# Kernel optimization log

Hardware: AMD Instinct MI355X
Metric: run time of the kernel (lower is better)

Reference implementation:

```python
import jax, jax.numpy as jnp
import numpy as np

jax.config.update("jax_enable_x64", True)

# --- static config (matches init_kwargs) ---
L = 6            # voxel_level_num
F = 8            # feature_dim
T = 524288       # per-level feature table size
B = 4194304      # buffer_size (hash table size)
N = 1048576      # number of query points
LEAF = 0.25      # leaf_voxel_size
UP = 2.0         # up_scale_factor

PRIMES = jnp.array([73856093, 19349669, 83492791], dtype=jnp.int64)
# corner offsets, z varies fastest (same order as torch self.steps)
STEPS = jnp.array([[0,0,0],[0,0,1],[0,1,0],[0,1,1],
                   [1,0,0],[1,0,1],[1,1,0],[1,1,1]], dtype=jnp.float32)


def setup_inputs() -> dict:
    key = jax.random.key(0)
    k1, k2, k3, k4 = jax.random.split(key, 4)
    query_points = jax.random.uniform(k1, (N, 3), dtype=jnp.float32) * 50.0
    features = 0.01 * jax.random.normal(k2, (L, T, F), dtype=jnp.float32)
    idx = jax.random.randint(k3, (L, B), 0, T, dtype=jnp.int64)
    empty = jax.random.uniform(k4, (L, B)) < 0.2
    feature_indexs = jnp.where(empty, jnp.int64(-1), idx)
    return {"query_points": query_points, "features": features,
            "feature_indexs": feature_indexs}


def _trilinear_coeffs(d):
    # d: [N,3] fractional coords in the cell; order matches STEPS (z fastest)
    tx, ty, tz = d[:, 0], d[:, 1], d[:, 2]
    return jnp.stack([
        (1-tx)*(1-ty)*(1-tz), (1-tx)*(1-ty)*tz,
        (1-tx)*ty*(1-tz),     (1-tx)*ty*tz,
        tx*(1-ty)*(1-tz),     tx*(1-ty)*tz,
        tx*ty*(1-tz),         tx*ty*tz,
    ], axis=1)  # [N,8]


def reference(query_points, features, feature_indexs):
    out = jnp.zeros((query_points.shape[0], F), dtype=query_points.dtype)
    for i in range(L):  # small fixed level loop (structurally distinct resolutions)
        res = LEAF * (UP ** i)
        scaled = query_points / res                      # [N,3]
        base = jnp.floor(scaled)
        corners = (base[:, None, :] + STEPS[None]).astype(jnp.int64)  # [N,8,3]
        keys = jnp.mod((corners * PRIMES).sum(-1), B)    # [N,8] spatial hash
        idx = feature_indexs[i][keys]                    # [N,8] gather, -1 = empty
        valid = idx.min(axis=1) > -1                     # [N] all 8 corners allocated
        coeffs = _trilinear_coeffs(scaled - base)        # [N,8]
        feats = features[i][jnp.clip(idx, 0, T - 1)]     # [N,8,F] gather
        level = jnp.einsum('nkf,nk->nf', feats, coeffs)  # trilinear interp
        out = out + jnp.where(valid[:, None], level, jnp.zeros((), out.dtype))
    return out
```

## Files before the change

### kernel.cpp

```cpp
#include <hip/hip_runtime.h>


static constexpr int      NPTS  = 1048576;
static constexpr int      LVLS  = 6;
static constexpr int      NF    = 8;
static constexpr int      TTAB  = 524288;
static constexpr unsigned BTAB  = 4194304u;
static constexpr unsigned BMASK = BTAB - 1u;
static constexpr unsigned P0 = 73856093u, P1 = 19349669u, P2 = 83492791u;

static constexpr int NBIN = 4096;
static constexpr int SB   = 256;
static constexpr int PPB  = NPTS / SB;
static constexpr int ITER = PPB / 256;
static constexpr int BCAP = 512;

typedef float f4 __attribute__((ext_vector_type(4)));

__device__ __forceinline__ void nhv_point(
    float qx, float qy, float qz,
    const float* __restrict__ feat, const int* __restrict__ fidx, float acc[NF])
{
    float    fx[LVLS], fy[LVLS], fz[LVLS];
    unsigned h[LVLS];
#pragma unroll
    for (int i = 0; i < LVLS; ++i) {
        const float inv = 4.0f / (float)(1 << i);
        const float sx = qx * inv, sy = qy * inv, sz = qz * inv;
        const float bx = floorf(sx), by = floorf(sy), bz = floorf(sz);
        fx[i] = sx - bx; fy[i] = sy - by; fz[i] = sz - bz;
        h[i] = (unsigned)(int)bx * P0 + (unsigned)(int)by * P1 + (unsigned)(int)bz * P2;
    }

    int id[LVLS][8];
#pragma unroll
    for (int i = 0; i < LVLS; ++i) {
        const int* __restrict__ tab = fidx + (size_t)i * BTAB;
#pragma unroll
        for (int k = 0; k < 8; ++k) {
            unsigned key = h[i];
            if (k & 4) key += P0;
            if (k & 2) key += P1;
            if (k & 1) key += P2;
            id[i][k] = tab[key & BMASK];
        }
    }

#pragma unroll
    for (int f = 0; f < NF; ++f) acc[f] = 0.0f;

#pragma unroll
    for (int i = 0; i < LVLS; ++i) {
        int mn = id[i][0];
#pragma unroll
        for (int k = 1; k < 8; ++k) mn = min(mn, id[i][k]);
        if (mn > -1) {
            const float wxv[2] = {1.0f - fx[i], fx[i]};
            const float wyv[2] = {1.0f - fy[i], fy[i]};
            const float wzv[2] = {1.0f - fz[i], fz[i]};
            const float* __restrict__ fb = feat + (size_t)i * (TTAB * NF);
#pragma unroll
            for (int k = 0; k < 8; ++k) {
                const float c = wxv[(k >> 2) & 1] * wyv[(k >> 1) & 1] * wzv[k & 1];
                const float4* p = (const float4*)(fb + (size_t)id[i][k] * NF);
                const float4 lo = p[0];
                const float4 hi = p[1];
                acc[0] += c * lo.x; acc[1] += c * lo.y;
                acc[2] += c * lo.z; acc[3] += c * lo.w;
                acc[4] += c * hi.x; acc[5] += c * hi.y;
                acc[6] += c * hi.z; acc[7] += c * hi.w;
            }
        }
    }
}

__device__ __forceinline__ unsigned expand4(unsigned v) {
    return (v & 1u) | ((v & 2u) << 2) | ((v & 4u) << 4) | ((v & 8u) << 6);
}
__device__ __forceinline__ unsigned bin_of(float x, float y, float z) {
    unsigned bx = min(15u, (unsigned)(int)(x * 0.32f));
    unsigned by = min(15u, (unsigned)(int)(y * 0.32f));
    unsigned bz = min(15u, (unsigned)(int)(z * 0.32f));
    return expand4(bx) | (expand4(by) << 1) | (expand4(bz) << 2);
}
__device__ __forceinline__ unsigned expand10(unsigned v) {
    v = (v | (v << 16)) & 0x030000FFu;
    v = (v | (v << 8))  & 0x0300F00Fu;
    v = (v | (v << 4))  & 0x030C30C3u;
    v = (v | (v << 2))  & 0x09249249u;
    return v;
}
__device__ __forceinline__ unsigned morton30(float x, float y, float z) {
    unsigned ux = min(1023u, (unsigned)(int)(x * 20.48f));
    unsigned uy = min(1023u, (unsigned)(int)(y * 20.48f));
    unsigned uz = min(1023u, (unsigned)(int)(z * 20.48f));
    return expand10(ux) | (expand10(uy) << 1) | (expand10(uz) << 2);
}

__global__ __launch_bounds__(256) void hist_k(const float* __restrict__ qp,
                                              unsigned* __restrict__ hist) {
    __shared__ unsigned lh[NBIN];
    const int b = blockIdx.x, t = threadIdx.x;
    for (int i = t; i < NBIN; i += 256) lh[i] = 0u;
    __syncthreads();
    const int base = b * PPB;
#pragma unroll
    for (int i = 0; i < ITER; ++i) {
        const int p = base + i * 256 + t;
        atomicAdd(&lh[bin_of(qp[3*p], qp[3*p+1], qp[3*p+2])], 1u);
    }
    __syncthreads();
    for (int i = t; i < NBIN; i += 256) hist[(size_t)b * NBIN + i] = lh[i];
}

__global__ __launch_bounds__(256) void colscan_k(unsigned* __restrict__ hist,
                                                 unsigned* __restrict__ binbase) {
    const int bin = blockIdx.x * 256 + threadIdx.x;
    unsigned run = 0;
    for (int b = 0; b < SB; ++b) {
        const unsigned v = hist[(size_t)b * NBIN + bin];
        hist[(size_t)b * NBIN + bin] = run;
        run += v;
    }
    binbase[bin] = run;
}

__global__ __launch_bounds__(256) void binscan_k(unsigned* __restrict__ binbase) {
    __shared__ unsigned tot[256];
    const int t = threadIdx.x;
    unsigned v[16];
    unsigned s = 0;
#pragma unroll
    for (int i = 0; i < 16; ++i) { v[i] = s; s += binbase[t * 16 + i]; }
    tot[t] = s;
    __syncthreads();
    for (int d = 1; d < 256; d <<= 1) {
        const unsigned x = (t >= d) ? tot[t - d] : 0u;
        __syncthreads();
        tot[t] += x;
        __syncthreads();
    }
    const unsigned cb = tot[t] - s;
#pragma unroll
    for (int i = 0; i < 16; ++i) binbase[t * 16 + i] = cb + v[i];
}

__global__ __launch_bounds__(256) void scatter_k(const float* __restrict__ qp,
                                                 const unsigned* __restrict__ hist,
                                                 const unsigned* __restrict__ binbase,
                                                 float4* __restrict__ sorted) {
    __shared__ unsigned cur[NBIN];
    const int b = blockIdx.x, t = threadIdx.x;
    for (int i = t; i < NBIN; i += 256)
        cur[i] = binbase[i] + hist[(size_t)b * NBIN + i];
    __syncthreads();
    const int base = b * PPB;
#pragma unroll
    for (int i = 0; i < ITER; ++i) {
        const int p = base + i * 256 + t;
        const float x = qp[3*p], y = qp[3*p+1], z = qp[3*p+2];
        const unsigned slot = atomicAdd(&cur[bin_of(x, y, z)], 1u);
        sorted[slot] = make_float4(x, y, z, __uint_as_float((unsigned)p));
    }
}

__global__ __launch_bounds__(256) void binsort_k(float4* __restrict__ sorted,
                                                 const unsigned* __restrict__ binbase) {
    __shared__ float4   pts[BCAP];
    __shared__ unsigned key[BCAP];
    __shared__ unsigned short pay[BCAP];

    const int bin   = blockIdx.x;
    const int t     = threadIdx.x;
    const unsigned start = binbase[bin];
    const unsigned end   = (bin < NBIN - 1) ? binbase[bin + 1] : (unsigned)NPTS;
    const int n = (int)(end - start);
    if (n <= 1 || n > BCAP) return;

#pragma unroll
    for (int r = 0; r < BCAP / 256; ++r) {
        const int i = r * 256 + t;
        if (i < n) {
            const float4 p = sorted[start + i];
            pts[i] = p;
            key[i] = morton30(p.x, p.y, p.z);
        } else {
            key[i] = 0xFFFFFFFFu;
        }
        pay[i] = (unsigned short)i;
    }
    __syncthreads();

    for (int k = 2; k <= BCAP; k <<= 1) {
        for (int j = k >> 1; j > 0; j >>= 1) {
#pragma unroll
            for (int r = 0; r < BCAP / 512; ++r) {
                const int tid = r * 256 + t;
                const int i   = ((tid & ~(j - 1)) << 1) | (tid & (j - 1));
                const int p2  = i | j;
                const bool up = ((i & k) == 0);
                const unsigned ka = key[i], kb = key[p2];
                if ((ka > kb) == up) {
                    key[i] = kb; key[p2] = ka;
                    const unsigned short tmp = pay[i]; pay[i] = pay[p2]; pay[p2] = tmp;
                }
            }
            __syncthreads();
        }
    }

#pragma unroll
    for (int r = 0; r < BCAP / 256; ++r) {
        const int i = r * 256 + t;
        if (i < n) sorted[start + i] = pts[pay[i]];
    }
}

__global__ __launch_bounds__(256) void nhv_sorted_k(
    const float4* __restrict__ sp, const float* __restrict__ feat,
    const int* __restrict__ fidx, float* __restrict__ out)
{
    const int nwg = NPTS / 256;
    const int bid = blockIdx.x;
    const int swz = (bid & 7) * (nwg >> 3) + (bid >> 3);
    const int j   = swz * 256 + (int)threadIdx.x;

    const f4 s = __builtin_nontemporal_load((const f4*)sp + j);
    float acc[NF];
    nhv_point(s.x, s.y, s.z, feat, fidx, acc);
    const unsigned n = __float_as_uint(s.w);

    f4* o = (f4*)(out + (size_t)n * NF);
    f4 lo = {acc[0], acc[1], acc[2], acc[3]};
    f4 hi = {acc[4], acc[5], acc[6], acc[7]};
    __builtin_nontemporal_store(lo, o);
    __builtin_nontemporal_store(hi, o + 1);
}

__global__ __launch_bounds__(256) void nhv_direct_k(
    const float* __restrict__ qp, const float* __restrict__ feat,
    const int* __restrict__ fidx, float* __restrict__ out)
{
    const int n = blockIdx.x * 256 + threadIdx.x;
    if (n >= NPTS) return;
    float acc[NF];
    nhv_point(qp[3*n], qp[3*n+1], qp[3*n+2], feat, fidx, acc);
    float4* o = (float4*)(out + (size_t)n * NF);
    o[0] = make_float4(acc[0], acc[1], acc[2], acc[3]);
    o[1] = make_float4(acc[4], acc[5], acc[6], acc[7]);
}

extern "C" void kernel_launch(void* const* d_in, const int* in_sizes, int n_in,
                              void* d_out, int out_size, void* d_ws, size_t ws_size,
                              hipStream_t stream) {
    const float* qp   = (const float*)d_in[0];
    const float* feat = (const float*)d_in[1];
    const int*   fidx = (const int*)d_in[2];
    float*       out  = (float*)d_out;

    const size_t ws_needed = (size_t)NPTS * 16;

    if (ws_size >= ws_needed) {
        unsigned* hist    = (unsigned*)d_out;
        unsigned* binbase = hist + (size_t)SB * NBIN;
        float4*   sorted  = (float4*)d_ws;

        hipLaunchKernelGGL(hist_k,    dim3(SB),   dim3(256), 0, stream, qp, hist);
        hipLaunchKernelGGL(colscan_k, dim3(16),   dim3(256), 0, stream, hist, binbase);
        hipLaunchKernelGGL(binscan_k, dim3(1),    dim3(256), 0, stream, binbase);
        hipLaunchKernelGGL(scatter_k, dim3(SB),   dim3(256), 0, stream, qp, hist, binbase, sorted);
        hipLaunchKernelGGL(binsort_k, dim3(NBIN), dim3(256), 0, stream, sorted, binbase);
        hipLaunchKernelGGL(nhv_sorted_k, dim3(NPTS/256), dim3(256), 0, stream,
                           sorted, feat, fidx, out);
    } else {
        hipLaunchKernelGGL(nhv_direct_k, dim3(NPTS/256), dim3(256), 0, stream,
                           qp, feat, fidx, out);
    }
}
```

Baseline: 223.9 us.

## Add validity bitmap prepass and replace bitonic bin sort with counting sort

A new kernel packs the per-level hash table's -1 markers into a bitmap, 32 slots per word, built freshly on every call. The main kernel first checks corner validity against this compact bitmap and fetches indices and features only for levels where all 8 corners are allocated. This cuts index-table traffic for invalid levels, at the cost of streaming the full 6x4M index table once to build the bitmap. The per-bin bitonic Morton sort is also replaced by a cheaper 64-way counting sort on a coarse octant key, which gives less precise spatial ordering.

```diff
diff --git a/kernel.cpp b/kernel.cpp
--- a/kernel.cpp
+++ b/kernel.cpp
@@ -15,11 +15,33 @@
 static constexpr int ITER = PPB / 256;
 static constexpr int BCAP = 512;
 
+static constexpr int    BMW_L        = BTAB / 32;
+static constexpr size_t SORTED_BYTES = (size_t)NPTS * 16;
+static constexpr size_t BM_BYTES     = (size_t)LVLS * BMW_L * 4;
+
 typedef float f4 __attribute__((ext_vector_type(4)));
-
-__device__ __forceinline__ void nhv_point(
+typedef int   i4 __attribute__((ext_vector_type(4)));
+
+__global__ __launch_bounds__(256) void bmbuild_k(const int* __restrict__ fidx,
+                                                 unsigned* __restrict__ bm) {
+    const int g = blockIdx.x * 256 + threadIdx.x;
+    const i4* p = (const i4*)(fidx + (size_t)g * 32);
+    unsigned w = 0;
+#pragma unroll
+    for (int j = 0; j < 8; ++j) {
+        const i4 v = __builtin_nontemporal_load(p + j);
+        w |= (unsigned)(v.x >= 0) << (4 * j + 0);
+        w |= (unsigned)(v.y >= 0) << (4 * j + 1);
+        w |= (unsigned)(v.z >= 0) << (4 * j + 2);
+        w |= (unsigned)(v.w >= 0) << (4 * j + 3);
+    }
+    bm[g] = w;
+}
+
+__device__ __forceinline__ void nhv_point_bm(
     float qx, float qy, float qz,
-    const float* __restrict__ feat, const int* __restrict__ fidx, float acc[NF])
+    const float* __restrict__ feat, const int* __restrict__ fidx,
+    const unsigned* __restrict__ bm, float acc[NF])
 {
     float    fx[LVLS], fy[LVLS], fz[LVLS];
     unsigned h[LVLS];
@@ -32,6 +54,72 @@
         h[i] = (unsigned)(int)bx * P0 + (unsigned)(int)by * P1 + (unsigned)(int)bz * P2;
     }
 
+    unsigned vmask = 0;
+#pragma unroll
+    for (int i = 0; i < LVLS; ++i) {
+        const unsigned* __restrict__ bl = bm + i * BMW_L;
+        unsigned v = ~0u;
+#pragma unroll
+        for (int k = 0; k < 8; ++k) {
+            unsigned key = h[i];
+            if (k & 4) key += P0;
+            if (k & 2) key += P1;
+            if (k & 1) key += P2;
+            key &= BMASK;
+            v &= (bl[key >> 5] >> (key & 31u));
+        }
+        vmask |= (v & 1u) << i;
+    }
+
+#pragma unroll
+    for (int f = 0; f < NF; ++f) acc[f] = 0.0f;
+
+#pragma unroll
+    for (int i = 0; i < LVLS; ++i) {
+        if (vmask & (1u << i)) {
+            const int* __restrict__ tab = fidx + (size_t)i * BTAB;
+            int id[8];
+#pragma unroll
+            for (int k = 0; k < 8; ++k) {
+                unsigned key = h[i];
+                if (k & 4) key += P0;
+                if (k & 2) key += P1;
+                if (k & 1) key += P2;
+                id[k] = tab[key & BMASK];
+            }
+            const float wxv[2] = {1.0f - fx[i], fx[i]};
+            const float wyv[2] = {1.0f - fy[i], fy[i]};
+            const float wzv[2] = {1.0f - fz[i], fz[i]};
+            const float* __restrict__ fb = feat + (size_t)i * (TTAB * NF);
+#pragma unroll
+            for (int k = 0; k < 8; ++k) {
+                const float c = wxv[(k >> 2) & 1] * wyv[(k >> 1) & 1] * wzv[k & 1];
+                const float4* p = (const float4*)(fb + (size_t)id[k] * NF);
+                const float4 lo = p[0];
+                const float4 hi = p[1];
+                acc[0] += c * lo.x; acc[1] += c * lo.y;
+                acc[2] += c * lo.z; acc[3] += c * lo.w;
+                acc[4] += c * hi.x; acc[5] += c * hi.y;
+                acc[6] += c * hi.z; acc[7] += c * hi.w;
+            }
+        }
+    }
+}
+
+__device__ __forceinline__ void nhv_point(
+    float qx, float qy, float qz,
+    const float* __restrict__ feat, const int* __restrict__ fidx, float acc[NF])
+{
+    float    fx[LVLS], fy[LVLS], fz[LVLS];
+    unsigned h[LVLS];
+#pragma unroll
+    for (int i = 0; i < LVLS; ++i) {
+        const float inv = 4.0f / (float)(1 << i);
+        const float sx = qx * inv, sy = qy * inv, sz = qz * inv;
+        const float bx = floorf(sx), by = floorf(sy), bz = floorf(sz);
+        fx[i] = sx - bx; fy[i] = sy - by; fz[i] = sz - bz;
+        h[i] = (unsigned)(int)bx * P0 + (unsigned)(int)by * P1 + (unsigned)(int)bz * P2;
+    }
     int id[LVLS][8];
 #pragma unroll
     for (int i = 0; i < LVLS; ++i) {
@@ -45,10 +133,8 @@
             id[i][k] = tab[key & BMASK];
         }
     }
-
 #pragma unroll
     for (int f = 0; f < NF; ++f) acc[f] = 0.0f;
-
 #pragma unroll
     for (int i = 0; i < LVLS; ++i) {
         int mn = id[i][0];
@@ -83,19 +169,6 @@
     unsigned bz = min(15u, (unsigned)(int)(z * 0.32f));
     return expand4(bx) | (expand4(by) << 1) | (expand4(bz) << 2);
 }
-__device__ __forceinline__ unsigned expand10(unsigned v) {
-    v = (v | (v << 16)) & 0x030000FFu;
-    v = (v | (v << 8))  & 0x0300F00Fu;
-    v = (v | (v << 4))  & 0x030C30C3u;
-    v = (v | (v << 2))  & 0x09249249u;
-    return v;
-}
-__device__ __forceinline__ unsigned morton30(float x, float y, float z) {
-    unsigned ux = min(1023u, (unsigned)(int)(x * 20.48f));
-    unsigned uy = min(1023u, (unsigned)(int)(y * 20.48f));
-    unsigned uz = min(1023u, (unsigned)(int)(z * 20.48f));
-    return expand10(ux) | (expand10(uy) << 1) | (expand10(uz) << 2);
-}
 
 __global__ __launch_bounds__(256) void hist_k(const float* __restrict__ qp,
                                               unsigned* __restrict__ hist) {
@@ -166,59 +239,54 @@
 
 __global__ __launch_bounds__(256) void binsort_k(float4* __restrict__ sorted,
                                                  const unsigned* __restrict__ binbase) {
-    __shared__ float4   pts[BCAP];
-    __shared__ unsigned key[BCAP];
-    __shared__ unsigned short pay[BCAP];
-
-    const int bin   = blockIdx.x;
-    const int t     = threadIdx.x;
+    __shared__ float4        pts[BCAP];
+    __shared__ unsigned char sk[BCAP];
+    __shared__ unsigned      cnt[64];
+
+    const int bin = blockIdx.x, t = threadIdx.x;
     const unsigned start = binbase[bin];
     const unsigned end   = (bin < NBIN - 1) ? binbase[bin + 1] : (unsigned)NPTS;
     const int n = (int)(end - start);
     if (n <= 1 || n > BCAP) return;
 
+    if (t < 64) cnt[t] = 0u;
+    __syncthreads();
 #pragma unroll
     for (int r = 0; r < BCAP / 256; ++r) {
         const int i = r * 256 + t;
         if (i < n) {
             const float4 p = sorted[start + i];
             pts[i] = p;
-            key[i] = morton30(p.x, p.y, p.z);
-        } else {
-            key[i] = 0xFFFFFFFFu;
-        }
-        pay[i] = (unsigned short)i;
-    }
-    __syncthreads();
-
-    for (int k = 2; k <= BCAP; k <<= 1) {
-        for (int j = k >> 1; j > 0; j >>= 1) {
-#pragma unroll
-            for (int r = 0; r < BCAP / 512; ++r) {
-                const int tid = r * 256 + t;
-                const int i   = ((tid & ~(j - 1)) << 1) | (tid & (j - 1));
-                const int p2  = i | j;
-                const bool up = ((i & k) == 0);
-                const unsigned ka = key[i], kb = key[p2];
-                if ((ka > kb) == up) {
-                    key[i] = kb; key[p2] = ka;
-                    const unsigned short tmp = pay[i]; pay[i] = pay[p2]; pay[p2] = tmp;
-                }
-            }
-            __syncthreads();
-        }
-    }
-
+            const unsigned ux = (unsigned)(int)(p.x * 1.28f) & 3u;
+            const unsigned uy = (unsigned)(int)(p.y * 1.28f) & 3u;
+            const unsigned uz = (unsigned)(int)(p.z * 1.28f) & 3u;
+            const unsigned s = (ux & 1u) | ((uy & 1u) << 1) | ((uz & 1u) << 2)
+                             | ((ux >> 1) << 3) | ((uy >> 1) << 4) | ((uz >> 1) << 5);
+            sk[i] = (unsigned char)s;
+            atomicAdd(&cnt[s], 1u);
+        }
+    }
+    __syncthreads();
+    if (t == 0) {
+        unsigned run = 0;
+#pragma unroll
+        for (int i = 0; i < 64; ++i) { const unsigned v = cnt[i]; cnt[i] = run; run += v; }
+    }
+    __syncthreads();
 #pragma unroll
     for (int r = 0; r < BCAP / 256; ++r) {
         const int i = r * 256 + t;
-        if (i < n) sorted[start + i] = pts[pay[i]];
-    }
-}
-
-__global__ __launch_bounds__(256) void nhv_sorted_k(
+        if (i < n) {
+            const unsigned dest = atomicAdd(&cnt[sk[i]], 1u);
+            sorted[start + dest] = pts[i];
+        }
+    }
+}
+
+__global__ __launch_bounds__(256) void nhv_sorted_bm_k(
     const float4* __restrict__ sp, const float* __restrict__ feat,
-    const int* __restrict__ fidx, float* __restrict__ out)
+    const int* __restrict__ fidx, const unsigned* __restrict__ bm,
+    float* __restrict__ out)
 {
     const int nwg = NPTS / 256;
     const int bid = blockIdx.x;
@@ -227,9 +295,29 @@
 
     const f4 s = __builtin_nontemporal_load((const f4*)sp + j);
     float acc[NF];
+    nhv_point_bm(s.x, s.y, s.z, feat, fidx, bm, acc);
+    const unsigned n = __float_as_uint(s.w);
+
+    f4* o = (f4*)(out + (size_t)n * NF);
+    f4 lo = {acc[0], acc[1], acc[2], acc[3]};
+    f4 hi = {acc[4], acc[5], acc[6], acc[7]};
+    __builtin_nontemporal_store(lo, o);
+    __builtin_nontemporal_store(hi, o + 1);
+}
+
+__global__ __launch_bounds__(256) void nhv_sorted_k(
+    const float4* __restrict__ sp, const float* __restrict__ feat,
+    const int* __restrict__ fidx, float* __restrict__ out)
+{
+    const int nwg = NPTS / 256;
+    const int bid = blockIdx.x;
+    const int swz = (bid & 7) * (nwg >> 3) + (bid >> 3);
+    const int j   = swz * 256 + (int)threadIdx.x;
+
+    const f4 s = __builtin_nontemporal_load((const f4*)sp + j);
+    float acc[NF];
     nhv_point(s.x, s.y, s.z, feat, fidx, acc);
     const unsigned n = __float_as_uint(s.w);
-
     f4* o = (f4*)(out + (size_t)n * NF);
     f4 lo = {acc[0], acc[1], acc[2], acc[3]};
     f4 hi = {acc[4], acc[5], acc[6], acc[7]};
@@ -258,13 +346,23 @@
     const int*   fidx = (const int*)d_in[2];
     float*       out  = (float*)d_out;
 
-    const size_t ws_needed = (size_t)NPTS * 16;
-
-    if (ws_size >= ws_needed) {
-        unsigned* hist    = (unsigned*)d_out;
-        unsigned* binbase = hist + (size_t)SB * NBIN;
-        float4*   sorted  = (float4*)d_ws;
-
+    unsigned* hist    = (unsigned*)d_out;
+    unsigned* binbase = hist + (size_t)SB * NBIN;
+
+    if (ws_size >= SORTED_BYTES + BM_BYTES) {
+        float4*   sorted = (float4*)d_ws;
+        unsigned* bm     = (unsigned*)((char*)d_ws + SORTED_BYTES);
+
+        hipLaunchKernelGGL(bmbuild_k, dim3(LVLS * BMW_L / 256), dim3(256), 0, stream, fidx, bm);
+        hipLaunchKernelGGL(hist_k,    dim3(SB),   dim3(256), 0, stream, qp, hist);
+        hipLaunchKernelGGL(colscan_k, dim3(16),   dim3(256), 0, stream, hist, binbase);
+        hipLaunchKernelGGL(binscan_k, dim3(1),    dim3(256), 0, stream, binbase);
+        hipLaunchKernelGGL(scatter_k, dim3(SB),   dim3(256), 0, stream, qp, hist, binbase, sorted);
+        hipLaunchKernelGGL(binsort_k, dim3(NBIN), dim3(256), 0, stream, sorted, binbase);
+        hipLaunchKernelGGL(nhv_sorted_bm_k, dim3(NPTS/256), dim3(256), 0, stream,
+                           sorted, feat, fidx, bm, out);
+    } else if (ws_size >= SORTED_BYTES) {
+        float4* sorted = (float4*)d_ws;
         hipLaunchKernelGGL(hist_k,    dim3(SB),   dim3(256), 0, stream, qp, hist);
         hipLaunchKernelGGL(colscan_k, dim3(16),   dim3(256), 0, stream, hist, binbase);
         hipLaunchKernelGGL(binscan_k, dim3(1),    dim3(256), 0, stream, binbase);
```

Result: slower. 229.8 us (+2.6%).
